# Performance work log

Hardware: AMD Instinct MI355X
Metric: run time of the kernel (lower is better)

The kernel has to match this reference:

```python
import jax, jax.numpy as jnp
import numpy as np

N = 50000      # nodes
E = 800000     # edges (avg degree 16)
IN = 128       # in_size
OUT = 64       # out_size
H = 32         # hidden_size
WIDTH = 3      # width
SCALE = 0.05


def _laplacian(x, src, tgt, n):
    # normalized Laplacian action: out[t] = sum_{edges into t} (x[t] - x[s]) / deg(t)
    deg = jax.ops.segment_sum(jnp.ones((tgt.shape[0],), x.dtype), tgt, num_segments=n)
    fac = 1.0 / deg[tgt]                       # [E], deg>=1 for any target that appears
    msg = (x[tgt] - x[src]) * fac[:, None]     # [E, F]
    return jax.ops.segment_sum(msg, tgt, num_segments=n)


def _grouped_linear(x, Wg, bg):
    # Conv1d(kernel=1, groups=width) == per-group linear
    n = x.shape[0]
    xg = x.reshape(n, WIDTH, -1)               # [N, width, h_in]
    out = jnp.einsum('nwh,who->nwo', xg, Wg) + bg
    return out.reshape(n, -1)                  # [N, width*h_out]


def setup_inputs() -> dict:
    key = jax.random.key(0)
    ks = jax.random.split(key, 14)
    data = jax.random.normal(ks[0], (N, IN), jnp.float32)
    src = jax.random.randint(ks[1], (E,), 0, N)
    tgt = jnp.sort(jax.random.randint(ks[2], (E,), 0, N))
    # preprocess ConvSkip: Linear(in, hidden*width) + Linear(in, hidden*width)
    W_pre = jax.random.normal(ks[3], (IN, H * WIDTH), jnp.float32) * SCALE
    b_pre = jnp.zeros((H * WIDTH,), jnp.float32)
    T_pre = jax.random.normal(ks[4], (IN, H * WIDTH), jnp.float32) * SCALE
    bT_pre = jnp.zeros((H * WIDTH,), jnp.float32)
    # middle WideConvSkip (depth-2 = 1 block): grouped conv [width, H, H]
    W_blk = jax.random.normal(ks[5], (WIDTH, H, H), jnp.float32) * SCALE
    b_blk = jnp.zeros((WIDTH, H), jnp.float32)
    T_blk = jax.random.normal(ks[6], (IN, H * WIDTH), jnp.float32) * SCALE
    bT_blk = jnp.zeros((H * WIDTH,), jnp.float32)
    # postprocess WideConvSkip: grouped conv [width, H, OUT]
    W_post = jax.random.normal(ks[7], (WIDTH, H, OUT), jnp.float32) * SCALE
    b_post = jnp.zeros((WIDTH, OUT), jnp.float32)
    T_post = jax.random.normal(ks[8], (IN, OUT * WIDTH), jnp.float32) * SCALE
    bT_post = jnp.zeros((OUT * WIDTH,), jnp.float32)
    return {"data": data, "src": src, "tgt": tgt,
            "W_pre": W_pre, "b_pre": b_pre, "T_pre": T_pre, "bT_pre": bT_pre,
            "W_blk": W_blk, "b_blk": b_blk, "T_blk": T_blk, "bT_blk": bT_blk,
            "W_post": W_post, "b_post": b_post, "T_post": T_post, "bT_post": bT_post}


def reference(data, src, tgt, W_pre, b_pre, T_pre, bT_pre,
              W_blk, b_blk, T_blk, bT_blk,
              W_post, b_post, T_post, bT_post):
    n = data.shape[0]
    # preprocess ConvSkip: sigma(L f(x) + g(x))
    out = data @ W_pre + b_pre
    out = _laplacian(out, src, tgt, n)
    out = jax.nn.relu(out + data @ T_pre + bT_pre)       # [N, H*width]
    # middle WideConvSkip (depth - 2 = 1)
    h = _grouped_linear(out, W_blk, b_blk)
    h = _laplacian(h, src, tgt, n)
    out = jax.nn.relu(h + data @ T_blk + bT_blk)          # [N, H*width]
    # postprocess WideConvSkip
    h = _grouped_linear(out, W_post, b_post)
    h = _laplacian(h, src, tgt, n)
    out = jax.nn.relu(h + data @ T_post + bT_post)        # [N, OUT*width]
    # reshape(N, -1, width) then adaptive_avg_pool1d(., 1) == mean over width
    out = out.reshape(n, -1, WIDTH)
    return out.mean(axis=-1, keepdims=True)               # [N, OUT, 1]
```

## Files before the change

### kernel.cpp

```cpp
#include <hip/hip_runtime.h>
#include <cstdint>
#include <cstddef>

#define N_NODES 50000
#define E_EDGES 800000
#define IN_F    128
#define PCOLS   512

typedef unsigned short ushortT;
typedef unsigned int   uintT;
typedef __attribute__((ext_vector_type(8))) short s8v;
typedef __attribute__((ext_vector_type(4))) float f4v;
typedef __attribute__((ext_vector_type(2))) float f2v;

__device__ __forceinline__ float bflo(uintT u){ union{uintT i;float f;}c; c.i=u<<16; return c.f; }
__device__ __forceinline__ float bfhi(uintT u){ union{uintT i;float f;}c; c.i=u&0xFFFF0000u; return c.f; }
__device__ __forceinline__ ushortT f2bfu(float f){
    union{float f;uintT u;}c; c.f=f;
    uintT r = c.u + 0x7FFF + ((c.u>>16)&1);
    return (ushortT)(r>>16);
}
__device__ __forceinline__ uintT pack2(float a, float b){
    return (uintT)f2bfu(a) | ((uintT)f2bfu(b) << 16);
}

__global__ void prep1(const float* __restrict__ A,
                      const float* __restrict__ Wp,  const float* __restrict__ bp,
                      const float* __restrict__ Tp,  const float* __restrict__ bTp,
                      const float* __restrict__ Tb,  const float* __restrict__ bTb,
                      const float* __restrict__ Tpo, const float* __restrict__ bTpo,
                      const float* __restrict__ Wpost,
                      const int* __restrict__ tgt,
                      ushortT* __restrict__ Wb, float* __restrict__ bcat,
                      float2* __restrict__ Wp2,
                      ushortT* __restrict__ Ab, int* __restrict__ row_ptr,
                      ushortT* __restrict__ Pb, ushortT* __restrict__ rb1,
                      ushortT* __restrict__ rb2)
{
    int gid = blockIdx.x * 256 + threadIdx.x;
    {
        size_t off = (size_t)gid * 8;
        float4 v0 = *(const float4*)(A + off);
        float4 v1 = *(const float4*)(A + off + 4);
        uint4 u;
        u.x = pack2(v0.x, v0.y); u.y = pack2(v0.z, v0.w);
        u.z = pack2(v1.x, v1.y); u.w = pack2(v1.z, v1.w);
        *(uint4*)(Ab + off) = u;
    }
    if (gid < IN_F * PCOLS) {
        int k = gid >> 9;
        int c = gid & 511;
        float v;
        if      (c < 96)  v = Wp [k*96  + c];
        else if (c < 192) v = Tp [k*96  + (c-96)];
        else if (c < 288) v = Tb [k*96  + (c-192)];
        else if (c < 480) v = Tpo[k*192 + (c-288)];
        else              v = 0.f;
        Wb[(size_t)c*IN_F + k] = f2bfu(v);
        if (k == 0) {
            float b;
            if      (c < 96)  b = bp  [c];
            else if (c < 192) b = bTp [c-96];
            else if (c < 288) b = bTb [c-192];
            else if (c < 480) b = bTpo[c-288];
            else              b = 0.f;
            bcat[c] = b;
        }
        if (gid < 3*16*64) {
            int w = gid >> 10, r = gid & 1023;
            int i2 = r >> 6, j = r & 63;
            Wp2[gid] = make_float2(Wpost[(w*32 + 2*i2)*64 + j],
                                   Wpost[(w*32 + 2*i2 + 1)*64 + j]);
        }
    }
    if (gid < 96) {
        Pb [(size_t)N_NODES*PCOLS + gid] = 0;
        rb1[(size_t)N_NODES*96   + gid] = 0;
        rb2[(size_t)N_NODES*96   + gid] = 0;
    }
    if (gid <= N_NODES) {
        int lo = 0, hi = E_EDGES;
        while (lo < hi) {
            int mid = (lo + hi) >> 1;
            if (tgt[mid] < gid) lo = mid + 1; else hi = mid;
        }
        row_ptr[gid] = lo;
    }
}

__global__ __launch_bounds__(256, 4) void gemm_mfma(const ushortT* __restrict__ Ab,
                                                    const ushortT* __restrict__ Wb,
                                                    const float* __restrict__ bcat,
                                                    ushortT* __restrict__ Pb, int M)
{
    __shared__ ushortT Bsl[128][136];
    int tid = threadIdx.x;
    int i = blockIdx.x;
    int xcd = i & 7, j = i >> 3;
    int nb = (j & 3) * 128;
    int mb = (xcd * 49 + (j >> 2)) * 128;
    int wv = tid >> 6, lane = tid & 63;
    int wm = wv >> 1, wn = wv & 1;
    int cl = lane & 15, q = lane >> 4;

    #pragma unroll
    for (int r = 0; r < 8; ++r) {
        int idx = tid + 256*r;
        int row = idx >> 4, qq = idx & 15;
        uint4 v = *(const uint4*)(Wb + (size_t)(nb+row)*IN_F + qq*8);
        *(uint4*)(&Bsl[row][qq*8]) = v;
    }
    __syncthreads();

    f4v acc[4][4];
    #pragma unroll
    for (int a = 0; a < 4; ++a)
        #pragma unroll
        for (int b = 0; b < 4; ++b) acc[a][b] = (f4v)0.f;

    int gmBase = mb + wm*64;
    #pragma unroll
    for (int ks = 0; ks < 4; ++ks) {
        int ko = ks*32 + q*8;
        s8v af[4], bf[4];
        #pragma unroll
        for (int mt = 0; mt < 4; ++mt) {
            int gm = gmBase + mt*16 + cl;
            uint4 va = make_uint4(0,0,0,0);
            if (gm < M) va = *(const uint4*)(Ab + (size_t)gm*IN_F + ko);
            af[mt] = *(s8v*)&va;
        }
        #pragma unroll
        for (int nt = 0; nt < 4; ++nt)
            bf[nt] = *(const s8v*)(&Bsl[wn*64 + nt*16 + cl][ko]);
        #pragma unroll
        for (int mt = 0; mt < 4; ++mt)
            #pragma unroll
            for (int nt = 0; nt < 4; ++nt)
                acc[mt][nt] = __builtin_amdgcn_mfma_f32_16x16x32_bf16(af[mt], bf[nt], acc[mt][nt], 0, 0, 0);
    }

    __syncthreads();

    #pragma unroll
    for (int nt = 0; nt < 4; ++nt) {
        int cn = wn*64 + nt*16 + cl;
        float bv = bcat[nb + cn];
        #pragma unroll
        for (int mt = 0; mt < 4; ++mt) {
            int rm0 = wm*64 + mt*16 + q*4;
            #pragma unroll
            for (int r = 0; r < 4; ++r)
                Bsl[rm0 + r][cn] = f2bfu(acc[mt][nt][r] + bv);
        }
    }
    __syncthreads();

    #pragma unroll
    for (int p = 0; p < 8; ++p) {
        int idx = tid + 256*p;
        int row = idx >> 4, sg = idx & 15;
        int gm = mb + row;
        if (gm < M) {
            uint4 v = *(const uint4*)(&Bsl[row][sg*8]);
            *(uint4*)(Pb + (size_t)gm*PCOLS + nb + sg*8) = v;
        }
    }
}

#define GATHER96(Xb, lo, deg, sv, pL, STRB, sx, sy)                               \
    float sx, sy;                                                                 \
    {                                                                             \
        f2v c0={0.f,0.f}, c1={0.f,0.f}, c2={0.f,0.f}, c3={0.f,0.f};               \
        int dmax = deg < 64 ? deg : 64;                                           \
        _Pragma("unroll 1")                                                       \
        for (int w_ = 0; w_ < dmax; w_ += 16) {                                   \
            uintT u[16];                                                          \
            _Pragma("unroll")                                                     \
            for (int kk = 0; kk < 16; ++kk) {                                     \
                int off = __builtin_amdgcn_readlane(sv, w_ + kk);                 \
                const char* rp = (const char*)(Xb) + off;                         \
                u[kk] = *(const uintT*)(rp + 4*pL);                               \
            }                                                                     \
            _Pragma("unroll")                                                     \
            for (int kk = 0; kk < 16; ++kk) {                                     \
                f2v v_; v_.x = bflo(u[kk]); v_.y = bfhi(u[kk]);                   \
                switch (kk & 3) {                                                 \
                    case 0: c0 += v_; break;                                      \
                    case 1: c1 += v_; break;                                      \
                    case 2: c2 += v_; break;                                      \
                    default:c3 += v_; break;                                      \
                }                                                                 \
            }                                                                     \
        }                                                                         \
        if (deg > 64) {                                                           \
            _Pragma("unroll 1")                                                   \
            for (int j_ = lo + 64; j_ < lo + deg; ++j_) {                         \
                int off = src[j_] * (STRB);                                       \
                const char* rp = (const char*)(Xb) + off;                         \
                uintT u0 = *(const uintT*)(rp + 4*pL);                            \
                f2v v_; v_.x = bflo(u0); v_.y = bfhi(u0);                         \
                c0 += v_;                                                         \
            }                                                                     \
        }                                                                         \
        f2v cs_ = (c0 + c1) + (c2 + c3);                                          \
        sx = cs_.x; sy = cs_.y;                                                   \
    }

#define MAKE_SV(lo, deg, lane, STRB, sv)                                          \
    int sv;                                                                       \
    {                                                                             \
        int e_ = (lo) + (lane);                                                   \
        if (e_ > E_EDGES - 1) e_ = E_EDGES - 1;                                   \
        int sn_ = src[e_];                                                        \
        sv = ((lane) < (deg) ? sn_ : N_NODES) * (STRB);                           \
    }

__global__ __launch_bounds__(256) void lap1(
    const ushortT* __restrict__ Pb,
    const int* __restrict__ src, const int* __restrict__ row_ptr,
    ushortT* __restrict__ rb1)
{
    int lane = threadIdx.x & 63;
    int t  = __builtin_amdgcn_readfirstlane((blockIdx.x << 2) + (threadIdx.x >> 6));
    int lo = __builtin_amdgcn_readfirstlane(row_ptr[t]);
    int deg = __builtin_amdgcn_readfirstlane(row_ptr[t+1]) - lo;
    int pL = lane < 48 ? lane : 0;
    MAKE_SV(lo, deg, lane, 2*PCOLS, sv)
    uintT ux = *(const uintT*)(Pb + (size_t)t*PCOLS + 2*pL);
    uintT zu = *(const uintT*)(Pb + (size_t)t*PCOLS + 96 + 2*pL);

    GATHER96(Pb, lo, deg, sv, pL, 2*PCOLS, sx, sy)

    float inv = deg > 0 ? 1.f/(float)deg : 0.f;
    float mf  = deg > 0 ? 1.f : 0.f;
    if (lane < 48) {
        float ox = fmaxf(mf*bflo(ux) - sx*inv + bflo(zu), 0.f);
        float oy = fmaxf(mf*bfhi(ux) - sy*inv + bfhi(zu), 0.f);
        *(uintT*)(rb1 + (size_t)t*96 + 2*pL) = pack2(ox, oy);
    }
}

__global__ __launch_bounds__(256) void lap2(
    const ushortT* __restrict__ Xb,
    const ushortT* __restrict__ Pb,
    const int* __restrict__ src, const int* __restrict__ row_ptr,
    const float* __restrict__ Wblk,
    ushortT* __restrict__ rb2)
{
    __shared__ float wS[3*32*32];
    for (int i = threadIdx.x; i < 3072; i += 256) wS[i] = Wblk[i];
    __syncthreads();

    int lane = threadIdx.x & 63;
    int wvw  = threadIdx.x >> 6;
    int pL = lane < 48 ? lane : 0;
    int w  = pL >> 4;
    int jj = pL & 15;
    const float2* wc = ((const float2*)wS) + (w*512 + jj);

    #pragma unroll 1
    for (int it = 0; it < 4; ++it) {
        int t  = __builtin_amdgcn_readfirstlane(blockIdx.x*16 + it*4 + wvw);
        int lo = __builtin_amdgcn_readfirstlane(row_ptr[t]);
        int deg = __builtin_amdgcn_readfirstlane(row_ptr[t+1]) - lo;
        MAKE_SV(lo, deg, lane, 192, sv)
        uintT ux = *(const uintT*)(Xb + (size_t)t*96 + 2*pL);
        uintT zu = *(const uintT*)(Pb + (size_t)t*PCOLS + 192 + 2*pL);

        GATHER96(Xb, lo, deg, sv, pL, 192, sx, sy)

        float inv = deg > 0 ? 1.f/(float)deg : 0.f;
        float mf  = deg > 0 ? 1.f : 0.f;
        float Lx = mf*bflo(ux) - sx*inv;
        float Ly = mf*bfhi(ux) - sy*inv;

        float accx = 0.f, accy = 0.f;
        #pragma unroll
        for (int d = 0; d < 16; ++d) {
            int sl = w*16 + d;
            float ax = __shfl(Lx, sl);
            float ay = __shfl(Ly, sl);
            float2 wa = wc[(2*d)*16];
            float2 wb = wc[(2*d+1)*16];
            accx = fmaf(ax, wa.x, accx); accx = fmaf(ay, wb.x, accx);
            accy = fmaf(ax, wa.y, accy); accy = fmaf(ay, wb.y, accy);
        }
        if (lane < 48) {
            float ox = fmaxf(accx + bflo(zu), 0.f);
            float oy = fmaxf(accy + bfhi(zu), 0.f);
            *(uintT*)(rb2 + (size_t)t*96 + 2*pL) = pack2(ox, oy);
        }
    }
}

__global__ __launch_bounds__(256) void lap3(
    const ushortT* __restrict__ Xb,
    const ushortT* __restrict__ Pb,
    const int* __restrict__ src, const int* __restrict__ row_ptr,
    const float2* __restrict__ Wp2,
    float* __restrict__ out)
{
    __shared__ float2 wS[3*16*64];
    __shared__ float  sm[4][96];
    for (int i = threadIdx.x; i < 3072; i += 256) wS[i] = Wp2[i];
    __syncthreads();

    int lane = threadIdx.x & 63;
    int wvw  = threadIdx.x >> 6;
    int pL = lane < 48 ? lane : 0;
    const float2* wl = wS + lane;

    #pragma unroll 1
    for (int it = 0; it < 4; ++it) {
        int t  = __builtin_amdgcn_readfirstlane(blockIdx.x*16 + it*4 + wvw);
        int lo = __builtin_amdgcn_readfirstlane(row_ptr[t]);
        int deg = __builtin_amdgcn_readfirstlane(row_ptr[t+1]) - lo;
        MAKE_SV(lo, deg, lane, 192, sv)
        uintT ux = *(const uintT*)(Xb + (size_t)t*96 + 2*pL);
        float z0 = bflo((uintT)Pb[(size_t)t*PCOLS + 288 + lane]);
        float z1 = bflo((uintT)Pb[(size_t)t*PCOLS + 352 + lane]);
        float z2 = bflo((uintT)Pb[(size_t)t*PCOLS + 416 + lane]);

        GATHER96(Xb, lo, deg, sv, pL, 192, sx, sy)

        float inv = deg > 0 ? 1.f/(float)deg : 0.f;
        float mf  = deg > 0 ? 1.f : 0.f;
        float Lx = mf*bflo(ux) - sx*inv;
        float Ly = mf*bfhi(ux) - sy*inv;

        if (lane < 48) {
            sm[wvw][2*pL]     = Lx;
            sm[wvw][2*pL + 1] = Ly;
        }
        __builtin_amdgcn_wave_barrier();

        float a0 = 0.f, a1 = 0.f, a2 = 0.f;
        #pragma unroll
        for (int w2 = 0; w2 < 3; ++w2) {
            float acc = 0.f;
            #pragma unroll
            for (int i2 = 0; i2 < 16; ++i2) {
                float2 iv = *(const float2*)(&sm[wvw][w2*32 + 2*i2]);
                float2 p  = wl[(w2*16 + i2)*64];
                acc = fmaf(iv.x, p.x, acc);
                acc = fmaf(iv.y, p.y, acc);
            }
            if (w2 == 0) a0 = acc; else if (w2 == 1) a1 = acc; else a2 = acc;
        }
        __builtin_amdgcn_wave_barrier();

        float o0 = fmaxf(a0 + z0, 0.f);
        float o1 = fmaxf(a1 + z1, 0.f);
        float o2 = fmaxf(a2 + z2, 0.f);
        float r = 0.f;
        #pragma unroll
        for (int q = 0; q < 3; ++q) {
            int c = 3*lane + q;
            int sl = c & 63, wsel = c >> 6;
            float v0 = __shfl(o0, sl);
            float v1 = __shfl(o1, sl);
            float v2 = __shfl(o2, sl);
            r += (wsel == 0) ? v0 : ((wsel == 1) ? v1 : v2);
        }
        out[(size_t)t*64 + lane] = r * (1.0f/3.0f);
    }
}

extern "C" void kernel_launch(void* const* d_in, const int* in_sizes, int n_in,
                              void* d_out, int out_size, void* d_ws, size_t ws_size,
                              hipStream_t stream)
{
    const float* data    = (const float*)d_in[0];
    const int*   src     = (const int*)  d_in[1];
    const int*   tgt     = (const int*)  d_in[2];
    const float* W_pre   = (const float*)d_in[3];
    const float* b_pre   = (const float*)d_in[4];
    const float* T_pre   = (const float*)d_in[5];
    const float* bT_pre  = (const float*)d_in[6];
    const float* W_blk   = (const float*)d_in[7];
    const float* b_blk   = (const float*)d_in[8];
    const float* T_blk   = (const float*)d_in[9];
    const float* bT_blk  = (const float*)d_in[10];
    const float* W_post  = (const float*)d_in[11];
    const float* b_post  = (const float*)d_in[12];
    const float* T_post  = (const float*)d_in[13];
    const float* bT_post = (const float*)d_in[14];
    float* out = (float*)d_out;

    float*   ws      = (float*)d_ws;
    float*   bcat    = ws;
    float2*  Wp2     = (float2*)(bcat + 512);
    int*     row_ptr = (int*)(Wp2 + 3*16*64);
    ushortT* Pb      = (ushortT*)(row_ptr + 50008);
    ushortT* rb1     = Pb  + (size_t)(N_NODES+1) * PCOLS;
    ushortT* rb2     = rb1 + (size_t)(N_NODES+1) * 96;
    ushortT* Ab      = rb2 + (size_t)(N_NODES+1) * 96;
    ushortT* Wb      = Ab  + (size_t)N_NODES * IN_F;

    prep1<<<(N_NODES*IN_F/8)/256, 256, 0, stream>>>(
        data, W_pre, b_pre, T_pre, bT_pre, T_blk, bT_blk, T_post, bT_post,
        W_post, tgt, Wb, bcat, Wp2, Ab, row_ptr, Pb, rb1, rb2);

    gemm_mfma<<<1568, 256, 0, stream>>>(Ab, Wb, bcat, Pb, N_NODES);

    lap1<<<N_NODES/4, 256, 0, stream>>>(Pb, src, row_ptr, rb1);
    lap2<<<N_NODES/16, 256, 0, stream>>>(rb1, Pb, src, row_ptr, W_blk, rb2);
    lap3<<<N_NODES/16, 256, 0, stream>>>(rb2, Pb, src, row_ptr, Wp2, out);
}
```

Measured before the change: 267.3 us.

## Gather two neighbor rows per wave with 8-byte loads and bpermute addressing

Rewrites the neighbor-gather macro so each wave splits into two 24-lane halves. Each half loads a different neighbor row using 8-byte loads, with row offsets distributed by ds_bpermute instead of readlane. Up to 48 neighbors are handled in two unrolled batches of 12, and the partial sums are recombined with shuffles. It also adds an occupancy hint of 8 to the launch bounds. The goal is fewer, wider memory instructions and more loads in flight per wave, at the cost of extra shuffles and a serial tail loop for degrees above 48.

```diff
diff --git a/kernel.cpp b/kernel.cpp
--- a/kernel.cpp
+++ b/kernel.cpp
@@ -168,43 +168,51 @@
     }
 }
 
-#define GATHER96(Xb, lo, deg, sv, pL, STRB, sx, sy)                               \
+#define ISSUE_W2(Xb, sv, bs, u)                                                   \
+    _Pragma("unroll")                                                             \
+    for (int s_ = 0; s_ < 12; ++s_) {                                             \
+        int vrow_ = __builtin_amdgcn_ds_bpermute(hb + ((bs) + s_)*8, sv);         \
+        u[s_] = *(const uint2*)((const char*)(Xb) + (uintT)(vrow_ + inner8));     \
+    }
+#define SUM_W2(u, p0, p1, q0, q1)                                                 \
+    _Pragma("unroll")                                                             \
+    for (int s_ = 0; s_ < 12; ++s_) {                                             \
+        f2v a_; a_.x = bflo(u[s_].x); a_.y = bfhi(u[s_].x);                       \
+        f2v b_; b_.x = bflo(u[s_].y); b_.y = bfhi(u[s_].y);                       \
+        if (s_ & 1) { p1 += a_; q1 += b_; } else { p0 += a_; q0 += b_; }          \
+    }
+#define GATHER2(Xb, lo, deg, sv, STRB, sx, sy)                                    \
     float sx, sy;                                                                 \
     {                                                                             \
-        f2v c0={0.f,0.f}, c1={0.f,0.f}, c2={0.f,0.f}, c3={0.f,0.f};               \
-        int dmax = deg < 64 ? deg : 64;                                           \
-        _Pragma("unroll 1")                                                       \
-        for (int w_ = 0; w_ < dmax; w_ += 16) {                                   \
-            uintT u[16];                                                          \
-            _Pragma("unroll")                                                     \
-            for (int kk = 0; kk < 16; ++kk) {                                     \
-                int off = __builtin_amdgcn_readlane(sv, w_ + kk);                 \
-                const char* rp = (const char*)(Xb) + off;                         \
-                u[kk] = *(const uintT*)(rp + 4*pL);                               \
-            }                                                                     \
-            _Pragma("unroll")                                                     \
-            for (int kk = 0; kk < 16; ++kk) {                                     \
-                f2v v_; v_.x = bflo(u[kk]); v_.y = bfhi(u[kk]);                   \
-                switch (kk & 3) {                                                 \
-                    case 0: c0 += v_; break;                                      \
-                    case 1: c1 += v_; break;                                      \
-                    case 2: c2 += v_; break;                                      \
-                    default:c3 += v_; break;                                      \
+        f2v p0={0.f,0.f}, p1={0.f,0.f}, q0={0.f,0.f}, q1={0.f,0.f};               \
+        uint2 u[12];                                                              \
+        ISSUE_W2(Xb, sv, 0, u)                                                    \
+        SUM_W2(u, p0, p1, q0, q1)                                                 \
+        if (deg > 24) {                                                           \
+            ISSUE_W2(Xb, sv, 12, u)                                               \
+            SUM_W2(u, p0, p1, q0, q1)                                             \
+        }                                                                         \
+        if (deg > 48) {                                                           \
+            _Pragma("unroll 1")                                                   \
+            for (int j_ = lo + 48; j_ < lo + deg; ++j_) {                         \
+                int off_ = src[j_] * (STRB);                                      \
+                uint2 t_ = *(const uint2*)((const char*)(Xb) + (uintT)(off_ + inner8)); \
+                if (lane < 24) {                                                  \
+                    f2v a_; a_.x = bflo(t_.x); a_.y = bfhi(t_.x);                 \
+                    f2v b_; b_.x = bflo(t_.y); b_.y = bfhi(t_.y);                 \
+                    p0 += a_; q0 += b_;                                           \
                 }                                                                 \
             }                                                                     \
         }                                                                         \
-        if (deg > 64) {                                                           \
-            _Pragma("unroll 1")                                                   \
-            for (int j_ = lo + 64; j_ < lo + deg; ++j_) {                         \
-                int off = src[j_] * (STRB);                                       \
-                const char* rp = (const char*)(Xb) + off;                         \
-                uintT u0 = *(const uintT*)(rp + 4*pL);                            \
-                f2v v_; v_.x = bflo(u0); v_.y = bfhi(u0);                         \
-                c0 += v_;                                                         \
-            }                                                                     \
-        }                                                                         \
-        f2v cs_ = (c0 + c1) + (c2 + c3);                                          \
-        sx = cs_.x; sy = cs_.y;                                                   \
+        f2v pt_ = p0 + p1, qt_ = q0 + q1;                                         \
+        int le_ = lane >> 1;                                                      \
+        float Ex_ = __shfl(pt_.x, le_),    Ey_ = __shfl(pt_.y, le_);              \
+        float Fx_ = __shfl(qt_.x, le_),    Fy_ = __shfl(qt_.y, le_);              \
+        float Gx_ = __shfl(pt_.x, le_+24), Gy_ = __shfl(pt_.y, le_+24);           \
+        float Hx_ = __shfl(qt_.x, le_+24), Hy_ = __shfl(qt_.y, le_+24);           \
+        bool od_ = (lane & 1);                                                    \
+        sx = (od_ ? Fx_ : Ex_) + (od_ ? Hx_ : Gx_);                               \
+        sy = (od_ ? Fy_ : Ey_) + (od_ ? Hy_ : Gy_);                               \
     }
 
 #define MAKE_SV(lo, deg, lane, STRB, sv)                                          \
@@ -216,21 +224,27 @@
         sv = ((lane) < (deg) ? sn_ : N_NODES) * (STRB);                           \
     }
 
-__global__ __launch_bounds__(256) void lap1(
+#define LANE_GEO                                                                  \
+    int lane = threadIdx.x & 63;                                                  \
+    int pL = lane < 48 ? lane : 0;                                                \
+    int lq = lane < 24 ? lane : (lane < 48 ? lane - 24 : 0);                      \
+    int hb = (lane >= 24 && lane < 48) ? 4 : 0;                                   \
+    int inner8 = lq * 8;
+
+__global__ __launch_bounds__(256, 8) void lap1(
     const ushortT* __restrict__ Pb,
     const int* __restrict__ src, const int* __restrict__ row_ptr,
     ushortT* __restrict__ rb1)
 {
-    int lane = threadIdx.x & 63;
+    LANE_GEO
     int t  = __builtin_amdgcn_readfirstlane((blockIdx.x << 2) + (threadIdx.x >> 6));
     int lo = __builtin_amdgcn_readfirstlane(row_ptr[t]);
     int deg = __builtin_amdgcn_readfirstlane(row_ptr[t+1]) - lo;
-    int pL = lane < 48 ? lane : 0;
     MAKE_SV(lo, deg, lane, 2*PCOLS, sv)
     uintT ux = *(const uintT*)(Pb + (size_t)t*PCOLS + 2*pL);
     uintT zu = *(const uintT*)(Pb + (size_t)t*PCOLS + 96 + 2*pL);
 
-    GATHER96(Pb, lo, deg, sv, pL, 2*PCOLS, sx, sy)
+    GATHER2(Pb, lo, deg, sv, 2*PCOLS, sx, sy)
 
     float inv = deg > 0 ? 1.f/(float)deg : 0.f;
     float mf  = deg > 0 ? 1.f : 0.f;
@@ -241,7 +255,7 @@
     }
 }
 
-__global__ __launch_bounds__(256) void lap2(
+__global__ __launch_bounds__(256, 8) void lap2(
     const ushortT* __restrict__ Xb,
     const ushortT* __restrict__ Pb,
     const int* __restrict__ src, const int* __restrict__ row_ptr,
@@ -252,9 +266,8 @@
     for (int i = threadIdx.x; i < 3072; i += 256) wS[i] = Wblk[i];
     __syncthreads();
 
-    int lane = threadIdx.x & 63;
+    LANE_GEO
     int wvw  = threadIdx.x >> 6;
-    int pL = lane < 48 ? lane : 0;
     int w  = pL >> 4;
     int jj = pL & 15;
     const float2* wc = ((const float2*)wS) + (w*512 + jj);
@@ -268,7 +281,7 @@
         uintT ux = *(const uintT*)(Xb + (size_t)t*96 + 2*pL);
         uintT zu = *(const uintT*)(Pb + (size_t)t*PCOLS + 192 + 2*pL);
 
-        GATHER96(Xb, lo, deg, sv, pL, 192, sx, sy)
+        GATHER2(Xb, lo, deg, sv, 192, sx, sy)
 
         float inv = deg > 0 ? 1.f/(float)deg : 0.f;
         float mf  = deg > 0 ? 1.f : 0.f;
@@ -294,7 +307,7 @@
     }
 }
 
-__global__ __launch_bounds__(256) void lap3(
+__global__ __launch_bounds__(256, 8) void lap3(
     const ushortT* __restrict__ Xb,
     const ushortT* __restrict__ Pb,
     const int* __restrict__ src, const int* __restrict__ row_ptr,
@@ -306,9 +319,8 @@
     for (int i = threadIdx.x; i < 3072; i += 256) wS[i] = Wp2[i];
     __syncthreads();
 
-    int lane = threadIdx.x & 63;
+    LANE_GEO
     int wvw  = threadIdx.x >> 6;
-    int pL = lane < 48 ? lane : 0;
     const float2* wl = wS + lane;
 
     #pragma unroll 1
@@ -322,7 +334,7 @@
         float z1 = bflo((uintT)Pb[(size_t)t*PCOLS + 352 + lane]);
         float z2 = bflo((uintT)Pb[(size_t)t*PCOLS + 416 + lane]);
 
-        GATHER96(Xb, lo, deg, sv, pL, 192, sx, sy)
+        GATHER2(Xb, lo, deg, sv, 192, sx, sy)
 
         float inv = deg > 0 ? 1.f/(float)deg : 0.f;
         float mf  = deg > 0 ? 1.f : 0.f;
```

New measurement: 319.8 us. 1.2x slower.

## Gather neighbor features from FP8 copies in all three Laplacian passes

Applied to the files above, without the earlier changes.

Adds FP8 (e4m3) shadow copies of the gathered feature matrices: a new conversion kernel turns the first GEMM output columns into FP8, and lap1/lap2 write FP8 copies of their outputs alongside the bf16 ones. All three Laplacian kernels now gather neighbor rows at 96 bytes per row instead of 192 or 1024, which cuts random-access gather traffic and improves cache hit rates. The cost is an extra kernel launch, extra stores, software FP8 decode, and a real loss of accuracy in the neighbor sums that may exceed tolerance.

```diff
diff --git a/kernel.cpp b/kernel.cpp
--- a/kernel.cpp
+++ b/kernel.cpp
@@ -1,4 +1,5 @@
 #include <hip/hip_runtime.h>
+#include <hip/hip_fp8.h>
 #include <cstdint>
 #include <cstddef>
 
@@ -9,6 +10,7 @@
 
 typedef unsigned short ushortT;
 typedef unsigned int   uintT;
+typedef unsigned char  u8T;
 typedef __attribute__((ext_vector_type(8))) short s8v;
 typedef __attribute__((ext_vector_type(4))) float f4v;
 typedef __attribute__((ext_vector_type(2))) float f2v;
@@ -22,6 +24,12 @@
 }
 __device__ __forceinline__ uintT pack2(float a, float b){
     return (uintT)f2bfu(a) | ((uintT)f2bfu(b) << 16);
+}
+__device__ __forceinline__ float f8f(uintT b){
+    __hip_fp8_e4m3 h; h.__x = (__hip_fp8_storage_t)(b & 0xFF); return (float)h;
+}
+__device__ __forceinline__ uintT ff8(float f){
+    __hip_fp8_e4m3 h(f); return (uintT)h.__x;
 }
 
 __global__ void prep1(const float* __restrict__ A,
@@ -34,8 +42,7 @@
                       ushortT* __restrict__ Wb, float* __restrict__ bcat,
                       float2* __restrict__ Wp2,
                       ushortT* __restrict__ Ab, int* __restrict__ row_ptr,
-                      ushortT* __restrict__ Pb, ushortT* __restrict__ rb1,
-                      ushortT* __restrict__ rb2)
+                      u8T* __restrict__ rb1f8, u8T* __restrict__ rb2f8)
 {
     int gid = blockIdx.x * 256 + threadIdx.x;
     {
@@ -73,10 +80,9 @@
                                    Wpost[(w*32 + 2*i2 + 1)*64 + j]);
         }
     }
-    if (gid < 96) {
-        Pb [(size_t)N_NODES*PCOLS + gid] = 0;
-        rb1[(size_t)N_NODES*96   + gid] = 0;
-        rb2[(size_t)N_NODES*96   + gid] = 0;
+    if (gid < 24) {
+        *(uintT*)(rb1f8 + (size_t)N_NODES*96 + 4*gid) = 0;
+        *(uintT*)(rb2f8 + (size_t)N_NODES*96 + 4*gid) = 0;
     }
     if (gid <= N_NODES) {
         int lo = 0, hi = E_EDGES;
@@ -168,7 +174,21 @@
     }
 }
 
-#define GATHER96(Xb, lo, deg, sv, pL, STRB, sx, sy)                               \
+__global__ void cvt_y0(const ushortT* __restrict__ Pb, u8T* __restrict__ Y8)
+{
+    int gid = blockIdx.x * 256 + threadIdx.x;
+    if (gid < N_NODES*24) {
+        int t = gid / 24, q = gid - t*24;
+        uint2 rv = *(const uint2*)(Pb + (size_t)t*PCOLS + 4*q);
+        uintT o = ff8(bflo(rv.x)) | (ff8(bfhi(rv.x)) << 8)
+                | (ff8(bflo(rv.y)) << 16) | (ff8(bfhi(rv.y)) << 24);
+        *(uintT*)(Y8 + (size_t)t*96 + 4*q) = o;
+    } else if (gid < N_NODES*24 + 24) {
+        *(uintT*)(Y8 + (size_t)N_NODES*96 + 4*(gid - N_NODES*24)) = 0;
+    }
+}
+
+#define GATHER96F8(X8, lo, deg, sv, pL, sx, sy)                                   \
     float sx, sy;                                                                 \
     {                                                                             \
         f2v c0={0.f,0.f}, c1={0.f,0.f}, c2={0.f,0.f}, c3={0.f,0.f};               \
@@ -179,12 +199,11 @@
             _Pragma("unroll")                                                     \
             for (int kk = 0; kk < 16; ++kk) {                                     \
                 int off = __builtin_amdgcn_readlane(sv, w_ + kk);                 \
-                const char* rp = (const char*)(Xb) + off;                         \
-                u[kk] = *(const uintT*)(rp + 4*pL);                               \
+                u[kk] = *(const ushortT*)((const u8T*)(X8) + off + 2*pL);         \
             }                                                                     \
             _Pragma("unroll")                                                     \
             for (int kk = 0; kk < 16; ++kk) {                                     \
-                f2v v_; v_.x = bflo(u[kk]); v_.y = bfhi(u[kk]);                   \
+                f2v v_; v_.x = f8f(u[kk]); v_.y = f8f(u[kk] >> 8);                \
                 switch (kk & 3) {                                                 \
                     case 0: c0 += v_; break;                                      \
                     case 1: c1 += v_; break;                                      \
@@ -196,10 +215,9 @@
         if (deg > 64) {                                                           \
             _Pragma("unroll 1")                                                   \
             for (int j_ = lo + 64; j_ < lo + deg; ++j_) {                         \
-                int off = src[j_] * (STRB);                                       \
-                const char* rp = (const char*)(Xb) + off;                         \
-                uintT u0 = *(const uintT*)(rp + 4*pL);                            \
-                f2v v_; v_.x = bflo(u0); v_.y = bfhi(u0);                         \
+                int off = src[j_] * 96;                                           \
+                uintT u0 = *(const ushortT*)((const u8T*)(X8) + off + 2*pL);      \
+                f2v v_; v_.x = f8f(u0); v_.y = f8f(u0 >> 8);                      \
                 c0 += v_;                                                         \
             }                                                                     \
         }                                                                         \
@@ -207,30 +225,31 @@
         sx = cs_.x; sy = cs_.y;                                                   \
     }
 
-#define MAKE_SV(lo, deg, lane, STRB, sv)                                          \
+#define MAKE_SV96(lo, deg, lane, sv)                                              \
     int sv;                                                                       \
     {                                                                             \
         int e_ = (lo) + (lane);                                                   \
         if (e_ > E_EDGES - 1) e_ = E_EDGES - 1;                                   \
         int sn_ = src[e_];                                                        \
-        sv = ((lane) < (deg) ? sn_ : N_NODES) * (STRB);                           \
+        sv = ((lane) < (deg) ? sn_ : N_NODES) * 96;                               \
     }
 
 __global__ __launch_bounds__(256) void lap1(
     const ushortT* __restrict__ Pb,
+    const u8T*     __restrict__ Y8,
     const int* __restrict__ src, const int* __restrict__ row_ptr,
-    ushortT* __restrict__ rb1)
+    ushortT* __restrict__ rb1, u8T* __restrict__ rb1f8)
 {
     int lane = threadIdx.x & 63;
     int t  = __builtin_amdgcn_readfirstlane((blockIdx.x << 2) + (threadIdx.x >> 6));
     int lo = __builtin_amdgcn_readfirstlane(row_ptr[t]);
     int deg = __builtin_amdgcn_readfirstlane(row_ptr[t+1]) - lo;
     int pL = lane < 48 ? lane : 0;
-    MAKE_SV(lo, deg, lane, 2*PCOLS, sv)
+    MAKE_SV96(lo, deg, lane, sv)
     uintT ux = *(const uintT*)(Pb + (size_t)t*PCOLS + 2*pL);
     uintT zu = *(const uintT*)(Pb + (size_t)t*PCOLS + 96 + 2*pL);
 
-    GATHER96(Pb, lo, deg, sv, pL, 2*PCOLS, sx, sy)
+    GATHER96F8(Y8, lo, deg, sv, pL, sx, sy)
 
     float inv = deg > 0 ? 1.f/(float)deg : 0.f;
     float mf  = deg > 0 ? 1.f : 0.f;
@@ -238,15 +257,17 @@
         float ox = fmaxf(mf*bflo(ux) - sx*inv + bflo(zu), 0.f);
         float oy = fmaxf(mf*bfhi(ux) - sy*inv + bfhi(zu), 0.f);
         *(uintT*)(rb1 + (size_t)t*96 + 2*pL) = pack2(ox, oy);
+        *(ushortT*)(rb1f8 + (size_t)t*96 + 2*pL) = (ushortT)(ff8(ox) | (ff8(oy) << 8));
     }
 }
 
 __global__ __launch_bounds__(256) void lap2(
     const ushortT* __restrict__ Xb,
+    const u8T*     __restrict__ X8,
     const ushortT* __restrict__ Pb,
     const int* __restrict__ src, const int* __restrict__ row_ptr,
     const float* __restrict__ Wblk,
-    ushortT* __restrict__ rb2)
+    ushortT* __restrict__ rb2, u8T* __restrict__ rb2f8)
 {
     __shared__ float wS[3*32*32];
     for (int i = threadIdx.x; i < 3072; i += 256) wS[i] = Wblk[i];
@@ -264,11 +285,11 @@
         int t  = __builtin_amdgcn_readfirstlane(blockIdx.x*16 + it*4 + wvw);
         int lo = __builtin_amdgcn_readfirstlane(row_ptr[t]);
         int deg = __builtin_amdgcn_readfirstlane(row_ptr[t+1]) - lo;
-        MAKE_SV(lo, deg, lane, 192, sv)
+        MAKE_SV96(lo, deg, lane, sv)
         uintT ux = *(const uintT*)(Xb + (size_t)t*96 + 2*pL);
         uintT zu = *(const uintT*)(Pb + (size_t)t*PCOLS + 192 + 2*pL);
 
-        GATHER96(Xb, lo, deg, sv, pL, 192, sx, sy)
+        GATHER96F8(X8, lo, deg, sv, pL, sx, sy)
 
         float inv = deg > 0 ? 1.f/(float)deg : 0.f;
         float mf  = deg > 0 ? 1.f : 0.f;
@@ -290,12 +311,14 @@
             float ox = fmaxf(accx + bflo(zu), 0.f);
             float oy = fmaxf(accy + bfhi(zu), 0.f);
             *(uintT*)(rb2 + (size_t)t*96 + 2*pL) = pack2(ox, oy);
+            *(ushortT*)(rb2f8 + (size_t)t*96 + 2*pL) = (ushortT)(ff8(ox) | (ff8(oy) << 8));
         }
     }
 }
 
 __global__ __launch_bounds__(256) void lap3(
     const ushortT* __restrict__ Xb,
+    const u8T*     __restrict__ X8,
     const ushortT* __restrict__ Pb,
     const int* __restrict__ src, const int* __restrict__ row_ptr,
     const float2* __restrict__ Wp2,
@@ -316,13 +339,13 @@
         int t  = __builtin_amdgcn_readfirstlane(blockIdx.x*16 + it*4 + wvw);
         int lo = __builtin_amdgcn_readfirstlane(row_ptr[t]);
         int deg = __builtin_amdgcn_readfirstlane(row_ptr[t+1]) - lo;
-        MAKE_SV(lo, deg, lane, 192, sv)
+        MAKE_SV96(lo, deg, lane, sv)
         uintT ux = *(const uintT*)(Xb + (size_t)t*96 + 2*pL);
         float z0 = bflo((uintT)Pb[(size_t)t*PCOLS + 288 + lane]);
         float z1 = bflo((uintT)Pb[(size_t)t*PCOLS + 352 + lane]);
         float z2 = bflo((uintT)Pb[(size_t)t*PCOLS + 416 + lane]);
 
-        GATHER96(Xb, lo, deg, sv, pL, 192, sx, sy)
+        GATHER96F8(X8, lo, deg, sv, pL, sx, sy)
 
         float inv = deg > 0 ? 1.f/(float)deg : 0.f;
         float mf  = deg > 0 ? 1.f : 0.f;
@@ -397,14 +420,19 @@
     ushortT* rb2     = rb1 + (size_t)(N_NODES+1) * 96;
     ushortT* Ab      = rb2 + (size_t)(N_NODES+1) * 96;
     ushortT* Wb      = Ab  + (size_t)N_NODES * IN_F;
+    u8T*     Y8      = (u8T*)(Wb + 512*IN_F);
+    u8T*     rb1f8   = Y8  + (size_t)(N_NODES+1) * 96;
+    u8T*     rb2f8   = rb1f8 + (size_t)(N_NODES+1) * 96;
 
     prep1<<<(N_NODES*IN_F/8)/256, 256, 0, stream>>>(
         data, W_pre, b_pre, T_pre, bT_pre, T_blk, bT_blk, T_post, bT_post,
-        W_post, tgt, Wb, bcat, Wp2, Ab, row_ptr, Pb, rb1, rb2);
+        W_post, tgt, Wb, bcat, Wp2, Ab, row_ptr, rb1f8, rb2f8);
 
     gemm_mfma<<<1568, 256, 0, stream>>>(Ab, Wb, bcat, Pb, N_NODES);
 
-    lap1<<<N_NODES/4, 256, 0, stream>>>(Pb, src, row_ptr, rb1);
-    lap2<<<N_NODES/16, 256, 0, stream>>>(rb1, Pb, src, row_ptr, W_blk, rb2);
-    lap3<<<N_NODES/16, 256, 0, stream>>>(rb2, Pb, src, row_ptr, Wp2, out);
-}
+    cvt_y0<<<(N_NODES*24 + 24 + 255)/256, 256, 0, stream>>>(Pb, Y8);
+
+    lap1<<<N_NODES/4, 256, 0, stream>>>(Pb, Y8, src, row_ptr, rb1, rb1f8);
+    lap2<<<N_NODES/16, 256, 0, stream>>>(rb1, rb1f8, Pb, src, row_ptr, W_blk, rb2, rb2f8);
+    lap3<<<N_NODES/16, 256, 0, stream>>>(rb2, rb2f8, Pb, src, row_ptr, Wp2, out);
+}
```

New measurement: 262.5 us. No clear change (-1.8%).
